# Kernel optimization log

Measured on AMD Instinct MI355X. Metric: run time of the kernel, lower is better.

The kernel has to match this reference:

```python
import jax, jax.numpy as jnp
import numpy as np

B, T, D = 1, 4096, 2048
H, HKV = 16, 4
DH = D // H            # 128
GROUP = H // HKV       # 4
ROPE_BASE = 10000.0


def setup_inputs() -> dict:
    key = jax.random.key(0)
    kx, kq, kk, kv, ko = jax.random.split(key, 5)
    s = 0.02
    return {
        "x": jax.random.normal(kx, (B, T, D), dtype=jnp.float32),
        "Wq": jax.random.normal(kq, (D, D), dtype=jnp.float32) * s,
        "Wk": jax.random.normal(kk, (D, HKV * DH), dtype=jnp.float32) * s,
        "Wv": jax.random.normal(kv, (D, HKV * DH), dtype=jnp.float32) * s,
        "Wo": jax.random.normal(ko, (D, D), dtype=jnp.float32) * s,
    }


def _rope_sincos(t, half):
    inv_freq = 1.0 / (ROPE_BASE ** (jnp.arange(half, dtype=jnp.float32) / half))
    ang = jnp.arange(t, dtype=jnp.float32)[:, None] * inv_freq  # [T, half]
    # broadcast over batch and head dims: [1, T, 1, half]
    return jnp.sin(ang)[None, :, None, :], jnp.cos(ang)[None, :, None, :]


def _apply_rope(x, sin, cos, half):
    x1, x2 = x[..., :half], x[..., half:]
    return jnp.concatenate([x1 * cos - x2 * sin, x1 * sin + x2 * cos], axis=-1)


def reference(x, Wq, Wk, Wv, Wo):
    b, t, d = x.shape
    q = (x @ Wq).reshape(b, t, H, DH)      # [B,T,H,Dh], H ordered (Hkv, group)
    k = (x @ Wk).reshape(b, t, HKV, DH)    # [B,T,Hkv,Dh]
    v = (x @ Wv).reshape(b, t, HKV, DH)

    half = DH // 2
    sin, cos = _rope_sincos(t, half)
    q = _apply_rope(q, sin, cos, half)
    k = _apply_rope(k, sin, cos, half)

    # GQA without materializing repeated K/V: split q heads into (kv_head, group)
    qg = q.reshape(b, t, HKV, GROUP, DH)
    att = jnp.einsum('bthgd,bshd->bhgts', qg, k) / np.float32(np.sqrt(DH))
    causal = jnp.tril(jnp.ones((t, t), dtype=bool))
    att = jnp.where(causal[None, None, None, :, :], att, -jnp.inf)
    att = jax.nn.softmax(att, axis=-1)
    y = jnp.einsum('bhgts,bshd->bthgd', att, v).reshape(b, t, d)
    return y @ Wo
```

## Files before the change

### kernel.cpp

```cpp
#include <hip/hip_runtime.h>
#include <hip/hip_bf16.h>

#define TT 4096
#define DD 2048
#define NH 16
#define NKV 4
#define DHD 128
#define NQKV 3072

typedef __attribute__((ext_vector_type(8))) short short8;
typedef __attribute__((ext_vector_type(4))) float f32x4;
typedef __hip_bfloat16 bf16;

#define GLOAD_LDS16(g, l)                                                \
    __builtin_amdgcn_global_load_lds(                                    \
        (const __attribute__((address_space(1))) unsigned int*)(g),      \
        (__attribute__((address_space(3))) unsigned int*)(l), 16, 0, 0)

__global__ void cast_x_kernel(const float* __restrict__ x, bf16* __restrict__ xb, int n) {
    int i = (blockIdx.x * blockDim.x + threadIdx.x) * 4;
    if (i >= n) return;
    float4 v = *(const float4*)(x + i);
    xb[i + 0] = __float2bfloat16(v.x);
    xb[i + 1] = __float2bfloat16(v.y);
    xb[i + 2] = __float2bfloat16(v.z);
    xb[i + 3] = __float2bfloat16(v.w);
}

__global__ void transpose_cast_all(const float* __restrict__ Wq, const float* __restrict__ Wk,
                                   const float* __restrict__ Wv, const float* __restrict__ Wo,
                                   bf16* __restrict__ Wt, bf16* __restrict__ Wot) {
    __shared__ float tile[32][33];
    const float* in;
    bf16* out;
    int N, rowOff;
    switch (blockIdx.z) {
        case 0: in = Wq; out = Wt; N = 2048; rowOff = 0; break;
        case 1: in = Wk; out = Wt; N = 512; rowOff = 2048; break;
        case 2: in = Wv; out = Wt; N = 512; rowOff = 2560; break;
        default: in = Wo; out = Wot; N = 2048; rowOff = 0; break;
    }
    int n0 = blockIdx.y * 32;
    if (n0 >= N) return;
    int k0 = blockIdx.x * 32;
    int tx = threadIdx.x, ty = threadIdx.y;
#pragma unroll
    for (int i = 0; i < 4; ++i)
        tile[ty + i * 8][tx] = in[(size_t)(k0 + ty + i * 8) * N + n0 + tx];
    __syncthreads();
#pragma unroll
    for (int i = 0; i < 4; ++i)
        out[(size_t)(rowOff + n0 + ty + i * 8) * 2048 + k0 + tx] = __float2bfloat16(tile[tx][ty + i * 8]);
}

template <bool OUT_BF16>
__global__ __launch_bounds__(256) void gemm_bt_kernel(const bf16* __restrict__ A,
                                                      const bf16* __restrict__ Bt,
                                                      void* __restrict__ C,
                                                      int M, int N, int K) {
    __shared__ bf16 As[128 * 32];
    __shared__ bf16 Bs[128 * 32];
    int bn0 = blockIdx.x * 128, bm0 = blockIdx.y * 128;
    int tid = threadIdx.x;
    int wave = tid >> 6, lane = tid & 63, quad = lane >> 4, l15 = lane & 15;
    int wm = (wave >> 1) * 64, wn = (wave & 1) * 64;

    int srow = wave * 32 + (lane >> 2);
    int scol = (lane & 3) * 8;
    const bf16* gA = A + (size_t)(bm0 + srow) * K + scol;
    const bf16* gB = Bt + (size_t)(bn0 + srow) * K + scol;
    bf16* lA = As + srow * 32 + scol;
    bf16* lB = Bs + srow * 32 + scol;

    f32x4 zero = {0.f, 0.f, 0.f, 0.f};
    f32x4 acc[4][4];
#pragma unroll
    for (int i = 0; i < 4; ++i)
#pragma unroll
        for (int j = 0; j < 4; ++j) acc[i][j] = zero;

    for (int k0 = 0; k0 < K; k0 += 32) {
        GLOAD_LDS16(gA + k0, lA);
        GLOAD_LDS16(gA + k0 + (size_t)16 * K, lA + 16 * 32);
        GLOAD_LDS16(gB + k0, lB);
        GLOAD_LDS16(gB + k0 + (size_t)16 * K, lB + 16 * 32);
        __syncthreads();
        short8 af[4], bfr[4];
#pragma unroll
        for (int i = 0; i < 4; ++i) af[i] = *(const short8*)&As[(wm + i * 16 + l15) * 32 + quad * 8];
#pragma unroll
        for (int j = 0; j < 4; ++j) bfr[j] = *(const short8*)&Bs[(wn + j * 16 + l15) * 32 + quad * 8];
#pragma unroll
        for (int i = 0; i < 4; ++i)
#pragma unroll
            for (int j = 0; j < 4; ++j)
                acc[i][j] = __builtin_amdgcn_mfma_f32_16x16x32_bf16(af[i], bfr[j], acc[i][j], 0, 0, 0);
        __syncthreads();
    }
#pragma unroll
    for (int i = 0; i < 4; ++i)
#pragma unroll
        for (int j = 0; j < 4; ++j)
#pragma unroll
            for (int r = 0; r < 4; ++r) {
                int row = bm0 + wm + i * 16 + quad * 4 + r;
                int col = bn0 + wn + j * 16 + l15;
                float v = acc[i][j][r];
                if (OUT_BF16)
                    ((bf16*)C)[(size_t)row * N + col] = __float2bfloat16(v);
                else
                    ((float*)C)[(size_t)row * N + col] = v;
            }
}

__global__ void rope_split_kernel(const bf16* __restrict__ QKV, bf16* __restrict__ Qs,
                                  bf16* __restrict__ Ks, bf16* __restrict__ Vt) {
    int slot = blockIdx.x * 4 + (threadIdx.x >> 6);
    int d = threadIdx.x & 63;
    int t = slot / 24, c = slot % 24;
    const bf16* base = QKV + (size_t)t * NQKV;
    int off = (c < 16) ? c * 128 : (c < 20) ? 2048 + (c - 16) * 128 : 2560 + (c - 20) * 128;
    float x1 = __bfloat162float(base[off + d]);
    float x2 = __bfloat162float(base[off + 64 + d]);
    float o1, o2;
    if (c < 20) {
        float invf = __expf((float)d * -0.14391156831f);
        float ang = (float)t * invf;
        float sn = sinf(ang), cs = cosf(ang);
        o1 = x1 * cs - x2 * sn;
        o2 = x1 * sn + x2 * cs;
    } else {
        o1 = x1;
        o2 = x2;
    }
    if (c < 16) {
        const float scale = 0.12751741f;
        o1 *= scale;
        o2 *= scale;
        bf16* dst = Qs + ((size_t)c * TT + t) * DHD;
        dst[d] = __float2bfloat16(o1);
        dst[d + 64] = __float2bfloat16(o2);
    } else if (c < 20) {
        bf16* dst = Ks + ((size_t)(c - 16) * TT + t) * DHD;
        dst[d] = __float2bfloat16(o1);
        dst[d + 64] = __float2bfloat16(o2);
    } else {
        int gg = c - 20;
        Vt[((size_t)gg * DHD + d) * TT + t] = __float2bfloat16(o1);
        Vt[((size_t)gg * DHD + d + 64) * TT + t] = __float2bfloat16(o2);
    }
}

__global__ __launch_bounds__(256, 4) void attn_kernel(const bf16* __restrict__ Qs,
                                                      const bf16* __restrict__ Ks,
                                                      const bf16* __restrict__ Vt,
                                                      bf16* __restrict__ Y) {
    __shared__ bf16 KsL[64 * 128];
    __shared__ bf16 VtL[128 * 64];
    __shared__ bf16 PsL[4][16 * 64];
    int h = blockIdx.y, bpair = blockIdx.x, g = h >> 2;
    int tid = threadIdx.x, wave = tid >> 6, lane = tid & 63, quad = lane >> 4, l15 = lane & 15;

    const bf16* kg = Ks + (size_t)g * TT * DHD;
    const bf16* vg = Vt + (size_t)g * DHD * TT;
    f32x4 zero = {0.f, 0.f, 0.f, 0.f};

    for (int pass = 0; pass < 2; ++pass) {
        int qt = (pass == 0) ? bpair : 63 - bpair;
        int qbase = qt * 64 + wave * 16;

        short8 qf[4];
        const bf16* qptr = Qs + ((size_t)h * TT + qbase + l15) * DHD + quad * 8;
#pragma unroll
        for (int ks = 0; ks < 4; ++ks) qf[ks] = *(const short8*)(qptr + ks * 32);

        f32x4 acc[8];
#pragma unroll
        for (int i = 0; i < 8; ++i) acc[i] = zero;
        float m_i = -1e30f, l_i = 0.f;

        for (int kt = 0; kt <= qt; ++kt) {
            int kb = kt * 64;
            bool diag = (kt == qt);
            short8 kv[4], vv[4];
            int krow[4], kc[4], vrow[4], vc[4];
#pragma unroll
            for (int r = 0; r < 4; ++r) {
                int idx = r * 256 + tid;
                krow[r] = idx >> 4;
                kc[r] = idx & 15;
                kv[r] = *(const short8*)(kg + (size_t)(kb + krow[r]) * DHD + kc[r] * 8);
                vrow[r] = idx >> 3;
                vc[r] = idx & 7;
                vv[r] = *(const short8*)(vg + (size_t)vrow[r] * TT + kb + vc[r] * 8);
            }
            __syncthreads();
#pragma unroll
            for (int r = 0; r < 4; ++r) {
                *(short8*)&KsL[krow[r] * 128 + ((kc[r] ^ (krow[r] & 15)) * 8)] = kv[r];
                *(short8*)&VtL[vrow[r] * 64 + ((vc[r] ^ (vrow[r] & 7)) * 8)] = vv[r];
            }
            __syncthreads();

            f32x4 s[4];
#pragma unroll
            for (int nt = 0; nt < 4; ++nt) {
                if (!diag || nt <= wave) {
                    s[nt] = zero;
#pragma unroll
                    for (int ks = 0; ks < 4; ++ks) {
                        int ch = (ks * 4 + quad) ^ l15;
                        short8 kf = *(const short8*)&KsL[(nt * 16 + l15) * 128 + ch * 8];
                        s[nt] = __builtin_amdgcn_mfma_f32_16x16x32_bf16(kf, qf[ks], s[nt], 0, 0, 0);
                    }
                    if (diag && nt == wave) {
#pragma unroll
                        for (int r = 0; r < 4; ++r)
                            if (quad * 4 + r > l15) s[nt][r] = -1e30f;
                    }
                } else {
#pragma unroll
                    for (int r = 0; r < 4; ++r) s[nt][r] = -1e30f;
                }
            }

            float mloc = -1e30f;
#pragma unroll
            for (int nt = 0; nt < 4; ++nt)
#pragma unroll
                for (int r = 0; r < 4; ++r) mloc = fmaxf(mloc, s[nt][r]);
            mloc = fmaxf(mloc, __shfl_xor(mloc, 16));
            mloc = fmaxf(mloc, __shfl_xor(mloc, 32));
            float mnew = fmaxf(m_i, mloc);
            float alpha = exp2f(m_i - mnew);
            m_i = mnew;
            float sl = 0.f;
#pragma unroll
            for (int nt = 0; nt < 4; ++nt)
#pragma unroll
                for (int r = 0; r < 4; ++r) {
                    s[nt][r] = exp2f(s[nt][r] - mnew);
                    sl += s[nt][r];
                }
            sl += __shfl_xor(sl, 16);
            sl += __shfl_xor(sl, 32);
            l_i = l_i * alpha + sl;
#pragma unroll
            for (int d8 = 0; d8 < 8; ++d8)
#pragma unroll
                for (int r = 0; r < 4; ++r) acc[d8][r] *= alpha;

#pragma unroll
            for (int nt = 0; nt < 4; ++nt)
#pragma unroll
                for (int rr = 0; rr < 2; ++rr) {
                    int col = nt * 16 + quad * 4 + rr * 2;
                    int ch = (col >> 3) ^ (l15 & 7);
                    __hip_bfloat162 pk;
                    pk.x = __float2bfloat16(s[nt][rr * 2]);
                    pk.y = __float2bfloat16(s[nt][rr * 2 + 1]);
                    *(__hip_bfloat162*)&PsL[wave][l15 * 64 + ch * 8 + (col & 7)] = pk;
                }
            asm volatile("s_waitcnt lgkmcnt(0)" ::: "memory");

            int kkmax = diag ? (wave >> 1) + 1 : 2;
#pragma unroll
            for (int kk = 0; kk < 2; ++kk) {
                if (kk < kkmax) {
                    int chp = (kk * 4 + quad) ^ (l15 & 7);
                    short8 pf = *(const short8*)&PsL[wave][l15 * 64 + chp * 8];
#pragma unroll
                    for (int d8 = 0; d8 < 8; ++d8) {
                        short8 vf = *(const short8*)&VtL[(d8 * 16 + l15) * 64 + chp * 8];
                        acc[d8] = __builtin_amdgcn_mfma_f32_16x16x32_bf16(vf, pf, acc[d8], 0, 0, 0);
                    }
                }
            }
        }

        float linv = 1.0f / l_i;
        __syncthreads();
        bf16* ow = KsL + wave * 2048;
#pragma unroll
        for (int d8 = 0; d8 < 8; ++d8)
#pragma unroll
            for (int rr = 0; rr < 2; ++rr) {
                int colD = d8 * 16 + quad * 4 + rr * 2;
                int ch = (colD >> 3) ^ (l15 & 7);
                __hip_bfloat162 o2;
                o2.x = __float2bfloat16(acc[d8][rr * 2] * linv);
                o2.y = __float2bfloat16(acc[d8][rr * 2 + 1] * linv);
                *(__hip_bfloat162*)&ow[l15 * 128 + ch * 8 + (colD & 7)] = o2;
            }
        asm volatile("s_waitcnt lgkmcnt(0)" ::: "memory");
#pragma unroll
        for (int c = 0; c < 4; ++c) {
            int chunk = quad * 4 + c;
            int ch = chunk ^ (l15 & 7);
            short8 ov = *(const short8*)&ow[l15 * 128 + ch * 8];
            *(short8*)&Y[(size_t)(qbase + l15) * DD + h * DHD + chunk * 8] = ov;
        }
        __syncthreads();
    }
}

extern "C" void kernel_launch(void* const* d_in, const int* in_sizes, int n_in,
                              void* d_out, int out_size, void* d_ws, size_t ws_size,
                              hipStream_t stream) {
    const float* x = (const float*)d_in[0];
    const float* Wq = (const float*)d_in[1];
    const float* Wk = (const float*)d_in[2];
    const float* Wv = (const float*)d_in[3];
    const float* Wo = (const float*)d_in[4];

    char* ws = (char*)d_ws;
    size_t off = 0;
    auto alloc = [&](size_t bytes) {
        void* p = ws + off;
        off += (bytes + 255) & ~(size_t)255;
        return p;
    };
    bf16* xb = (bf16*)alloc((size_t)TT * DD * 2);
    bf16* Wt = (bf16*)alloc((size_t)NQKV * DD * 2);
    bf16* Wot = (bf16*)alloc((size_t)DD * DD * 2);
    bf16* QKVb = (bf16*)alloc((size_t)TT * NQKV * 2);
    bf16* Qs = (bf16*)alloc((size_t)NH * TT * DHD * 2);
    bf16* Ksb = (bf16*)alloc((size_t)NKV * TT * DHD * 2);
    bf16* Vtb = (bf16*)alloc((size_t)NKV * DHD * TT * 2);
    bf16* Yb = (bf16*)alloc((size_t)TT * DD * 2);

    cast_x_kernel<<<(TT * DD / 4 + 255) / 256, 256, 0, stream>>>(x, xb, TT * DD);
    transpose_cast_all<<<dim3(64, 64, 4), dim3(32, 8), 0, stream>>>(Wq, Wk, Wv, Wo, Wt, Wot);

    gemm_bt_kernel<true><<<dim3(NQKV / 128, TT / 128), 256, 0, stream>>>(xb, Wt, QKVb, TT, NQKV, DD);
    rope_split_kernel<<<TT * 24 / 4, 256, 0, stream>>>(QKVb, Qs, Ksb, Vtb);
    attn_kernel<<<dim3(32, NH), 256, 0, stream>>>(Qs, Ksb, Vtb, Yb);
    gemm_bt_kernel<false><<<dim3(DD / 128, TT / 128), 256, 0, stream>>>(Yb, Wot, d_out, TT, DD, DD);
}
```

Measured before the change: 420.5 us.

## Use 128-key tiles with register prefetch of next K/V tile in attention

The attention kernel now processes keys in 128-wide tiles instead of 64, doubling LDS buffers. Global loads for the next K/V tile are issued into registers right after the current tile is staged in LDS, so they overlap with the MFMA and softmax work. The trailing barrier per pass is dropped and the swizzle patterns are adjusted for the wider tiles. This should halve barrier and loop overhead per key and hide load latency, at the cost of more LDS and registers (occupancy hint removed) and wasted work on half-masked diagonal tiles.

```diff
diff --git a/kernel.cpp b/kernel.cpp
--- a/kernel.cpp
+++ b/kernel.cpp
@@ -151,13 +151,13 @@
     }
 }
 
-__global__ __launch_bounds__(256, 4) void attn_kernel(const bf16* __restrict__ Qs,
-                                                      const bf16* __restrict__ Ks,
-                                                      const bf16* __restrict__ Vt,
-                                                      bf16* __restrict__ Y) {
-    __shared__ bf16 KsL[64 * 128];
-    __shared__ bf16 VtL[128 * 64];
-    __shared__ bf16 PsL[4][16 * 64];
+__global__ __launch_bounds__(256) void attn_kernel(const bf16* __restrict__ Qs,
+                                                   const bf16* __restrict__ Ks,
+                                                   const bf16* __restrict__ Vt,
+                                                   bf16* __restrict__ Y) {
+    __shared__ bf16 KsL[128 * 128];
+    __shared__ bf16 VtL[128 * 128];
+    __shared__ bf16 PsL[4][16 * 128];
     int h = blockIdx.y, bpair = blockIdx.x, g = h >> 2;
     int tid = threadIdx.x, wave = tid >> 6, lane = tid & 63, quad = lane >> 4, l15 = lane & 15;
 
@@ -165,9 +165,18 @@
     const bf16* vg = Vt + (size_t)g * DHD * TT;
     f32x4 zero = {0.f, 0.f, 0.f, 0.f};
 
+    int krow[8], kc[8];
+#pragma unroll
+    for (int r = 0; r < 8; ++r) {
+        int idx = r * 256 + tid;
+        krow[r] = idx >> 4;
+        kc[r] = idx & 15;
+    }
+
     for (int pass = 0; pass < 2; ++pass) {
         int qt = (pass == 0) ? bpair : 63 - bpair;
         int qbase = qt * 64 + wave * 16;
+        int ntiles = (qt + 2) >> 1;
 
         short8 qf[4];
         const bf16* qptr = Qs + ((size_t)h * TT + qbase + l15) * DHD + quad * 8;
@@ -179,33 +188,37 @@
         for (int i = 0; i < 8; ++i) acc[i] = zero;
         float m_i = -1e30f, l_i = 0.f;
 
-        for (int kt = 0; kt <= qt; ++kt) {
-            int kb = kt * 64;
-            bool diag = (kt == qt);
-            short8 kv[4], vv[4];
-            int krow[4], kc[4], vrow[4], vc[4];
-#pragma unroll
-            for (int r = 0; r < 4; ++r) {
-                int idx = r * 256 + tid;
-                krow[r] = idx >> 4;
-                kc[r] = idx & 15;
-                kv[r] = *(const short8*)(kg + (size_t)(kb + krow[r]) * DHD + kc[r] * 8);
-                vrow[r] = idx >> 3;
-                vc[r] = idx & 7;
-                vv[r] = *(const short8*)(vg + (size_t)vrow[r] * TT + kb + vc[r] * 8);
-            }
+        short8 kv[8], vv[8];
+#pragma unroll
+        for (int r = 0; r < 8; ++r) {
+            kv[r] = *(const short8*)(kg + (size_t)krow[r] * DHD + kc[r] * 8);
+            vv[r] = *(const short8*)(vg + (size_t)krow[r] * TT + kc[r] * 8);
+        }
+
+        for (int kt = 0; kt < ntiles; ++kt) {
             __syncthreads();
 #pragma unroll
-            for (int r = 0; r < 4; ++r) {
+            for (int r = 0; r < 8; ++r) {
                 *(short8*)&KsL[krow[r] * 128 + ((kc[r] ^ (krow[r] & 15)) * 8)] = kv[r];
-                *(short8*)&VtL[vrow[r] * 64 + ((vc[r] ^ (vrow[r] & 7)) * 8)] = vv[r];
+                *(short8*)&VtL[krow[r] * 128 + ((kc[r] ^ (krow[r] & 15)) * 8)] = vv[r];
             }
             __syncthreads();
 
-            f32x4 s[4];
-#pragma unroll
-            for (int nt = 0; nt < 4; ++nt) {
-                if (!diag || nt <= wave) {
+            int knext = (kt + 1 < ntiles) ? (kt + 1) * 128 : kt * 128;
+#pragma unroll
+            for (int r = 0; r < 8; ++r) {
+                kv[r] = *(const short8*)(kg + (size_t)(knext + krow[r]) * DHD + kc[r] * 8);
+                vv[r] = *(const short8*)(vg + (size_t)krow[r] * TT + knext + kc[r] * 8);
+            }
+
+            f32x4 s[8];
+#pragma unroll
+            for (int nt = 0; nt < 8; ++nt) {
+                int gsub = 2 * kt + (nt >> 2);
+                int nt4 = nt & 3;
+                bool full = (gsub < qt) || (gsub == qt && nt4 < wave);
+                bool dg = (gsub == qt && nt4 == wave);
+                if (full || dg) {
                     s[nt] = zero;
 #pragma unroll
                     for (int ks = 0; ks < 4; ++ks) {
@@ -213,7 +226,7 @@
                         short8 kf = *(const short8*)&KsL[(nt * 16 + l15) * 128 + ch * 8];
                         s[nt] = __builtin_amdgcn_mfma_f32_16x16x32_bf16(kf, qf[ks], s[nt], 0, 0, 0);
                     }
-                    if (diag && nt == wave) {
+                    if (dg) {
 #pragma unroll
                         for (int r = 0; r < 4; ++r)
                             if (quad * 4 + r > l15) s[nt][r] = -1e30f;
@@ -226,7 +239,7 @@
 
             float mloc = -1e30f;
 #pragma unroll
-            for (int nt = 0; nt < 4; ++nt)
+            for (int nt = 0; nt < 8; ++nt)
 #pragma unroll
                 for (int r = 0; r < 4; ++r) mloc = fmaxf(mloc, s[nt][r]);
             mloc = fmaxf(mloc, __shfl_xor(mloc, 16));
@@ -236,7 +249,7 @@
             m_i = mnew;
             float sl = 0.f;
 #pragma unroll
-            for (int nt = 0; nt < 4; ++nt)
+            for (int nt = 0; nt < 8; ++nt)
 #pragma unroll
                 for (int r = 0; r < 4; ++r) {
                     s[nt][r] = exp2f(s[nt][r] - mnew);
@@ -251,27 +264,29 @@
                 for (int r = 0; r < 4; ++r) acc[d8][r] *= alpha;
 
 #pragma unroll
-            for (int nt = 0; nt < 4; ++nt)
+            for (int nt = 0; nt < 8; ++nt)
 #pragma unroll
                 for (int rr = 0; rr < 2; ++rr) {
                     int col = nt * 16 + quad * 4 + rr * 2;
-                    int ch = (col >> 3) ^ (l15 & 7);
+                    int ch = (col >> 3) ^ l15;
                     __hip_bfloat162 pk;
                     pk.x = __float2bfloat16(s[nt][rr * 2]);
                     pk.y = __float2bfloat16(s[nt][rr * 2 + 1]);
-                    *(__hip_bfloat162*)&PsL[wave][l15 * 64 + ch * 8 + (col & 7)] = pk;
+                    *(__hip_bfloat162*)&PsL[wave][l15 * 128 + ch * 8 + (col & 7)] = pk;
                 }
             asm volatile("s_waitcnt lgkmcnt(0)" ::: "memory");
 
-            int kkmax = diag ? (wave >> 1) + 1 : 2;
-#pragma unroll
-            for (int kk = 0; kk < 2; ++kk) {
+            int rel = qt * 64 + wave * 16 + 15 - kt * 128;
+            int kkmax = min(4, (rel >> 5) + 1);
+#pragma unroll
+            for (int kk = 0; kk < 4; ++kk) {
                 if (kk < kkmax) {
-                    int chp = (kk * 4 + quad) ^ (l15 & 7);
-                    short8 pf = *(const short8*)&PsL[wave][l15 * 64 + chp * 8];
+                    int chp = (kk * 4 + quad) ^ l15;
+                    short8 pf = *(const short8*)&PsL[wave][l15 * 128 + chp * 8];
 #pragma unroll
                     for (int d8 = 0; d8 < 8; ++d8) {
-                        short8 vf = *(const short8*)&VtL[(d8 * 16 + l15) * 64 + chp * 8];
+                        int chv = (kk * 4 + quad) ^ l15;
+                        short8 vf = *(const short8*)&VtL[(d8 * 16 + l15) * 128 + chv * 8];
                         acc[d8] = __builtin_amdgcn_mfma_f32_16x16x32_bf16(vf, pf, acc[d8], 0, 0, 0);
                     }
                 }
@@ -286,21 +301,20 @@
 #pragma unroll
             for (int rr = 0; rr < 2; ++rr) {
                 int colD = d8 * 16 + quad * 4 + rr * 2;
-                int ch = (colD >> 3) ^ (l15 & 7);
+                int ch = (colD >> 4) ^ (l15 & 7);
                 __hip_bfloat162 o2;
                 o2.x = __float2bfloat16(acc[d8][rr * 2] * linv);
                 o2.y = __float2bfloat16(acc[d8][rr * 2 + 1] * linv);
-                *(__hip_bfloat162*)&ow[l15 * 128 + ch * 8 + (colD & 7)] = o2;
+                *(__hip_bfloat162*)&ow[l15 * 128 + ch * 16 + ((colD >> 3) & 1) * 8 + (colD & 7)] = o2;
             }
         asm volatile("s_waitcnt lgkmcnt(0)" ::: "memory");
 #pragma unroll
         for (int c = 0; c < 4; ++c) {
             int chunk = quad * 4 + c;
-            int ch = chunk ^ (l15 & 7);
-            short8 ov = *(const short8*)&ow[l15 * 128 + ch * 8];
+            int ch = (chunk >> 1) ^ (l15 & 7);
+            short8 ov = *(const short8*)&ow[l15 * 128 + ch * 16 + (chunk & 1) * 8];
             *(short8*)&Y[(size_t)(qbase + l15) * DD + h * DHD + chunk * 8] = ov;
         }
-        __syncthreads();
     }
 }
 
```

Measured after the change: 527.4 us. 1.25x slower.
